# Optimization experiments

Measured on AMD Instinct MI355X. Metric: run time of the kernel, lower is better.

Reference implementation:

```python
import jax, jax.numpy as jnp
import numpy as np

D = 10          # tree depth (perfect binary tree, heap layout)
K = 2           # MAX_CHILD
N = 2 ** D - 1  # nodes per tree = 1023
LD = 256        # latent_dim
B = 128         # batch of trees


def setup_inputs() -> dict:
    key = jax.random.key(0)
    ks = jax.random.split(key, 24)
    p = lambda k, shape: (jax.random.normal(k, shape, jnp.float32) * 0.05)
    return {
        "x_embed": jax.random.normal(ks[0], (B, N, LD), jnp.float32),
        "init_embedding": jax.random.normal(ks[1], (B, LD), jnp.float32),
        # leaf gates cx, ox
        "Wcx": p(ks[2], (LD, LD)), "bcx": p(ks[3], (LD,)),
        "Wox": p(ks[4], (LD, LD)), "box": p(ks[5], (LD,)),
        # token-input gates ix, fx, ux
        "Wix": p(ks[6], (LD, LD)), "bix": p(ks[7], (LD,)),
        "Wfx": p(ks[8], (LD, LD)), "bfx": p(ks[9], (LD,)),
        "Wux": p(ks[10], (LD, LD)), "bux": p(ks[11], (LD,)),
        # per-child gates: i_gates[K], f_gates[K][K], u_gates[K]
        "Wi": p(ks[12], (K, LD, LD)), "bi": p(ks[13], (K, LD)),
        "Wf": p(ks[14], (K, K, LD, LD)), "bf": p(ks[15], (K, K, LD)),
        "Wu": p(ks[16], (K, LD, LD)), "bu": p(ks[17], (K, LD)),
        # output projection oend: Linear(3*latent_dim, latent_dim)
        "Woend": p(ks[18], (3 * LD, LD)), "boend": p(ks[19], (LD,)),
    }


def _tree_lstm(x_embed, Wcx, bcx, Wox, box, Wix, bix, Wfx, bfx, Wux, bux,
               Wi, bi, Wf, bf, Wu, bu):
    lin = lambda x, W, b: x @ W + b
    # --- leaves (deepest level): c = cx(x); h = sigmoid(ox(x)) * tanh(c) ---
    leaf_start = 2 ** (D - 1) - 1
    x_leaf = x_embed[:, leaf_start:]                       # [B, 2^(D-1), d]
    c_leaf = lin(x_leaf, Wcx, bcx)
    h_leaf = jax.nn.sigmoid(lin(x_leaf, Wox, box)) * jnp.tanh(c_leaf)
    c_all = jnp.zeros_like(x_embed).at[:, leaf_start:].set(c_leaf)
    h_all = jnp.zeros_like(x_embed).at[:, leaf_start:].set(h_leaf)
    # --- internal levels, bottom-up (fixed D-1 iterations, vectorized over B*width) ---
    for lvl in range(D - 2, -1, -1):
        s, e = 2 ** lvl - 1, 2 ** (lvl + 1) - 1
        idx = np.arange(s, e)
        ch = np.stack([2 * idx + 1, 2 * idx + 2], axis=1)  # [w, K] heap children
        hch = h_all[:, ch]                                 # [B, w, K, d]
        cch = c_all[:, ch]                                 # [B, w, K, d]
        x = x_embed[:, s:e]                                # [B, w, d]
        # i = sigmoid(ix(x) + sum_k i_gates[k](h_k))
        i = jax.nn.sigmoid(lin(x, Wix, bix)
                           + jnp.einsum('bwkd,kde->bwe', hch, Wi) + bi.sum(0))
        # f_vals[k] = fx(x) + sum_j f_gates[k][j](h_j)   (NO sigmoid, faithful to source)
        f = (lin(x, Wfx, bfx)[:, :, None, :]
             + jnp.einsum('bwjd,kjde->bwke', hch, Wf) + bf.sum(1))   # [B, w, K, d]
        # u = tanh(ux(x) + sum_k u_gates[k](h_k))
        u = jnp.tanh(lin(x, Wux, bux)
                     + jnp.einsum('bwkd,kde->bwe', hch, Wu) + bu.sum(0))
        c = i * u + jnp.sum(f * cch, axis=2)
        h = jnp.tanh(c)
        c_all = c_all.at[:, s:e].set(c)
        h_all = h_all.at[:, s:e].set(h)
    return c_all[:, 0], h_all[:, 0]                        # root state (c, h)


def reference(x_embed, init_embedding, Wcx, bcx, Wox, box, Wix, bix, Wfx, bfx,
              Wux, bux, Wi, bi, Wf, bf, Wu, bu, Woend, boend):
    c_root, h_root = _tree_lstm(x_embed, Wcx, bcx, Wox, box, Wix, bix,
                                Wfx, bfx, Wux, bux, Wi, bi, Wf, bf, Wu, bu)
    s = jnp.concatenate([init_embedding, c_root, h_root], axis=1)  # [B, 3d]
    return jnp.tanh(s @ Woend + boend)                             # [B, d]
```

## Files before the change

### kernel.cpp

```cpp
#include <hip/hip_runtime.h>
#include <hip/hip_bf16.h>
#include <math.h>


#define NNODES 1023
#define BATCH  128
#define LDIM   256

typedef __attribute__((ext_vector_type(8))) short short8;
typedef __attribute__((ext_vector_type(4))) float f32x4;

__device__ __forceinline__ float sigmoidf_(float x) {
    return 1.f / (1.f + expf(-x));
}

__device__ __forceinline__ void split3(float x, ushort& h, ushort& m, ushort& l) {
    unsigned u = __float_as_uint(x);
    unsigned hu = (u + 0x7FFFu + ((u >> 16) & 1u)) & 0xFFFF0000u;
    h = (ushort)(hu >> 16);
    float r = x - __uint_as_float(hu);
    unsigned ur = __float_as_uint(r);
    unsigned mu = (ur + 0x7FFFu + ((ur >> 16) & 1u)) & 0xFFFF0000u;
    m = (ushort)(mu >> 16);
    float r2 = r - __uint_as_float(mu);
    unsigned u2 = __float_as_uint(r2);
    l = (ushort)((u2 + 0x7FFFu + ((u2 >> 16) & 1u)) >> 16);
}

__device__ __forceinline__ unsigned cvt_pk_bf16(float lo, float hi) {
    unsigned r;
    asm("v_cvt_pk_bf16_f32 %0, %1, %2" : "=v"(r) : "v"(lo), "v"(hi));
    return r;
}

struct P3 { unsigned h, m, l; };
__device__ __forceinline__ P3 pack2v(float x0, float x1) {
    P3 p;
    p.h = cvt_pk_bf16(x0, x1);
    float h0 = __uint_as_float(p.h << 16);
    float h1 = __uint_as_float(p.h & 0xFFFF0000u);
    float r0 = x0 - h0, r1 = x1 - h1;
    p.m = cvt_pk_bf16(r0, r1);
    float m0 = __uint_as_float(p.m << 16);
    float m1 = __uint_as_float(p.m & 0xFFFF0000u);
    p.l = cvt_pk_bf16(r0 - m0, r1 - m1);
    return p;
}

__global__ __launch_bounds__(256) void build_weights(
    const float* __restrict__ Wix, const float* __restrict__ bix,
    const float* __restrict__ Wfx, const float* __restrict__ bfx,
    const float* __restrict__ Wux, const float* __restrict__ bux,
    const float* __restrict__ Wi,  const float* __restrict__ bi,
    const float* __restrict__ Wf,  const float* __restrict__ bf,
    const float* __restrict__ Wu,  const float* __restrict__ bu,
    const float* __restrict__ Wcx, const float* __restrict__ bcx,
    const float* __restrict__ Wox, const float* __restrict__ box,
    float* __restrict__ Wbig, float* __restrict__ bias_big,
    float* __restrict__ Wleaf, float* __restrict__ bias_leaf)
{
    int i = blockIdx.x * blockDim.x + threadIdx.x;
    if (i < 768 * 1024) {
        int k = i >> 10, n = i & 1023;
        int g = n >> 8, nn = n & 255;
        float v;
        if (g == 0) {
            v = (k < 256) ? Wix[k * 256 + nn]
              : (k < 512) ? Wi[(k - 256) * 256 + nn]
                          : Wi[65536 + (k - 512) * 256 + nn];
        } else if (g == 1) {
            v = (k < 256) ? Wux[k * 256 + nn]
              : (k < 512) ? Wu[(k - 256) * 256 + nn]
                          : Wu[65536 + (k - 512) * 256 + nn];
        } else {
            int kf = g - 2;
            v = (k < 256) ? Wfx[k * 256 + nn]
              : (k < 512) ? Wf[((kf * 2 + 0) * 256 + (k - 256)) * 256 + nn]
                          : Wf[((kf * 2 + 1) * 256 + (k - 512)) * 256 + nn];
        }
        Wbig[i] = v;
        return;
    }
    i -= 768 * 1024;
    if (i < 1024) {
        int g = i >> 8, nn = i & 255;
        float v;
        if (g == 0)      v = bix[nn] + bi[nn] + bi[256 + nn];
        else if (g == 1) v = bux[nn] + bu[nn] + bu[256 + nn];
        else if (g == 2) v = bfx[nn] + bf[nn] + bf[256 + nn];
        else             v = bfx[nn] + bf[512 + nn] + bf[768 + nn];
        bias_big[i] = v;
        return;
    }
    i -= 1024;
    if (i < 256 * 512) {
        int k = i >> 9, n = i & 511;
        Wleaf[i] = (n < 256) ? Wcx[k * 256 + n] : Wox[k * 256 + (n - 256)];
        return;
    }
    i -= 256 * 512;
    if (i < 512) {
        bias_leaf[i] = (i < 256) ? bcx[i] : box[i - 256];
    }
}

__global__ __launch_bounds__(256) void split_weights_T(
    const float* __restrict__ Wbig,
    ushort* __restrict__ Wth, ushort* __restrict__ Wtm, ushort* __restrict__ Wtl)
{
    __shared__ float sh[32][33];
    const int k0 = blockIdx.x * 32, n0 = blockIdx.y * 32;
    const int t = threadIdx.x;
    {
        int r = t >> 3, c4 = (t & 7) * 4;
        float4 v = *(const float4*)&Wbig[(size_t)(k0 + r) * 1024 + n0 + c4];
        sh[r][c4] = v.x; sh[r][c4 + 1] = v.y; sh[r][c4 + 2] = v.z; sh[r][c4 + 3] = v.w;
    }
    __syncthreads();
    int n = t >> 3, kc = (t & 7) * 4;
    ushort oh[4], om[4], ol[4];
#pragma unroll
    for (int j = 0; j < 4; ++j)
        split3(sh[kc + j][n], oh[j], om[j], ol[j]);
    size_t o = (size_t)(n0 + n) * 768 + k0 + kc;
    *(ushort4*)&Wth[o] = make_ushort4(oh[0], oh[1], oh[2], oh[3]);
    *(ushort4*)&Wtm[o] = make_ushort4(om[0], om[1], om[2], om[3]);
    *(ushort4*)&Wtl[o] = make_ushort4(ol[0], ol[1], ol[2], ol[3]);
}

__global__ __launch_bounds__(256) void split_wleaf_T(
    const float* __restrict__ Wleaf,
    ushort* __restrict__ Lth, ushort* __restrict__ Ltm, ushort* __restrict__ Ltl)
{
    __shared__ float sh[32][33];
    const int k0 = blockIdx.x * 32, n0 = blockIdx.y * 32;
    const int t = threadIdx.x;
    {
        int r = t >> 3, c4 = (t & 7) * 4;
        float4 v = *(const float4*)&Wleaf[(size_t)(k0 + r) * 512 + n0 + c4];
        sh[r][c4] = v.x; sh[r][c4 + 1] = v.y; sh[r][c4 + 2] = v.z; sh[r][c4 + 3] = v.w;
    }
    __syncthreads();
    int n = t >> 3, kc = (t & 7) * 4;
    ushort oh[4], om[4], ol[4];
#pragma unroll
    for (int j = 0; j < 4; ++j)
        split3(sh[kc + j][n], oh[j], om[j], ol[j]);
    size_t o = (size_t)(n0 + n) * 256 + k0 + kc;
    *(ushort4*)&Lth[o] = make_ushort4(oh[0], oh[1], oh[2], oh[3]);
    *(ushort4*)&Ltm[o] = make_ushort4(om[0], om[1], om[2], om[3]);
    *(ushort4*)&Ltl[o] = make_ushort4(ol[0], ol[1], ol[2], ol[3]);
}

__global__ __launch_bounds__(256, 2) void mfma_level_pack(
    const float* __restrict__ x_embed,
    const float* __restrict__ hChild, const float* __restrict__ cChild,
    const ushort* __restrict__ Wth, const ushort* __restrict__ Wtm,
    const ushort* __restrict__ Wtl,
    const float* __restrict__ bias,
    float* __restrict__ hOut, float* __restrict__ cOut, int nstart)
{
    constexpr int AST = 40;
    __shared__ __align__(16) ushort Wlds[3][128 * AST];
    __shared__ __align__(16) ushort Vlds[3][128 * AST];

    const int tid  = threadIdx.x;
    const int node = blockIdx.x;
    const int gy   = blockIdx.y;
    const int lane = tid & 63, wid = tid >> 6;
    const int ni = wid & 1, bw = wid >> 1;
    const int srow = tid & 127, shalf = tid >> 7;

    const float* aX = x_embed + ((size_t)srow * NNODES + (nstart + node)) * LDIM;
    const float* aL = hChild + ((size_t)(2 * node) * BATCH + srow) * LDIM;
    const float* aR = aL + (size_t)BATCH * LDIM;
    const size_t nb = (size_t)(((srow >> 5) << 8) + gy * 32 + (srow & 31)) * 768;
    const ushort* w0 = Wth + nb;
    const ushort* w1 = Wtm + nb;
    const ushort* w2 = Wtl + nb;

    f32x4 acc[4][4];
#pragma unroll
    for (int g = 0; g < 4; ++g)
#pragma unroll
        for (int t2 = 0; t2 < 4; ++t2) acc[g][t2] = (f32x4){0.f, 0.f, 0.f, 0.f};

    float4 a0, a1, a2, a3;
    int4 w00, w01, w10, w11, w20, w21;

#define TREE_LOADS(IT)                                                         \
    {                                                                          \
        const int seg_  = (IT) >> 3;                                           \
        const int koff_ = ((IT) & 7) * 32 + shalf * 16;                        \
        const float* ap_ = (seg_ == 0) ? aX : (seg_ == 1) ? aL : aR;           \
        ap_ += koff_;                                                          \
        a0 = *(const float4*)(ap_);                                            \
        a1 = *(const float4*)(ap_ + 4);                                        \
        a2 = *(const float4*)(ap_ + 8);                                        \
        a3 = *(const float4*)(ap_ + 12);                                       \
        const int bko_ = (IT) * 32 + shalf * 16;                               \
        w00 = *(const int4*)(w0 + bko_); w01 = *(const int4*)(w0 + bko_ + 8);  \
        w10 = *(const int4*)(w1 + bko_); w11 = *(const int4*)(w1 + bko_ + 8);  \
        w20 = *(const int4*)(w2 + bko_); w21 = *(const int4*)(w2 + bko_ + 8);  \
    }

    TREE_LOADS(0);
    for (int it = 0; it < 24; ++it) {
        if (it) __syncthreads();
        {
            P3 p0 = pack2v(a0.x, a0.y), p1 = pack2v(a0.z, a0.w);
            P3 p2 = pack2v(a1.x, a1.y), p3 = pack2v(a1.z, a1.w);
            P3 p4 = pack2v(a2.x, a2.y), p5 = pack2v(a2.z, a2.w);
            P3 p6 = pack2v(a3.x, a3.y), p7 = pack2v(a3.z, a3.w);
            const int base = srow * AST + shalf * 16;
            *(int4*)&Vlds[0][base]     = make_int4((int)p0.h, (int)p1.h, (int)p2.h, (int)p3.h);
            *(int4*)&Vlds[0][base + 8] = make_int4((int)p4.h, (int)p5.h, (int)p6.h, (int)p7.h);
            *(int4*)&Vlds[1][base]     = make_int4((int)p0.m, (int)p1.m, (int)p2.m, (int)p3.m);
            *(int4*)&Vlds[1][base + 8] = make_int4((int)p4.m, (int)p5.m, (int)p6.m, (int)p7.m);
            *(int4*)&Vlds[2][base]     = make_int4((int)p0.l, (int)p1.l, (int)p2.l, (int)p3.l);
            *(int4*)&Vlds[2][base + 8] = make_int4((int)p4.l, (int)p5.l, (int)p6.l, (int)p7.l);
            *(int4*)&Wlds[0][base]     = w00;
            *(int4*)&Wlds[0][base + 8] = w01;
            *(int4*)&Wlds[1][base]     = w10;
            *(int4*)&Wlds[1][base + 8] = w11;
            *(int4*)&Wlds[2][base]     = w20;
            *(int4*)&Wlds[2][base + 8] = w21;
        }
        __syncthreads();
        if (it + 1 < 24) TREE_LOADS(it + 1);
        {
            short8 vf[4][3];
#pragma unroll
            for (int Nt = 0; Nt < 4; ++Nt) {
                const int rb = (bw * 64 + Nt * 16 + (lane & 15)) * AST + (lane >> 4) * 8;
#pragma unroll
                for (int s = 0; s < 3; ++s) vf[Nt][s] = *(const short8*)&Vlds[s][rb];
            }
#pragma unroll
            for (int g = 0; g < 4; ++g) {
                const int cb = (g * 32 + ni * 16 + (lane & 15)) * AST + (lane >> 4) * 8;
                short8 wh = *(const short8*)&Wlds[0][cb];
                short8 wm = *(const short8*)&Wlds[1][cb];
                short8 wl = *(const short8*)&Wlds[2][cb];
#pragma unroll
                for (int Nt = 0; Nt < 4; ++Nt)
                    acc[g][Nt] = __builtin_amdgcn_mfma_f32_16x16x32_bf16(wl, vf[Nt][0], acc[g][Nt], 0, 0, 0);
#pragma unroll
                for (int Nt = 0; Nt < 4; ++Nt)
                    acc[g][Nt] = __builtin_amdgcn_mfma_f32_16x16x32_bf16(wh, vf[Nt][2], acc[g][Nt], 0, 0, 0);
#pragma unroll
                for (int Nt = 0; Nt < 4; ++Nt)
                    acc[g][Nt] = __builtin_amdgcn_mfma_f32_16x16x32_bf16(wm, vf[Nt][1], acc[g][Nt], 0, 0, 0);
#pragma unroll
                for (int Nt = 0; Nt < 4; ++Nt)
                    acc[g][Nt] = __builtin_amdgcn_mfma_f32_16x16x32_bf16(wm, vf[Nt][0], acc[g][Nt], 0, 0, 0);
#pragma unroll
                for (int Nt = 0; Nt < 4; ++Nt)
                    acc[g][Nt] = __builtin_amdgcn_mfma_f32_16x16x32_bf16(wh, vf[Nt][1], acc[g][Nt], 0, 0, 0);
#pragma unroll
                for (int Nt = 0; Nt < 4; ++Nt)
                    acc[g][Nt] = __builtin_amdgcn_mfma_f32_16x16x32_bf16(wh, vf[Nt][0], acc[g][Nt], 0, 0, 0);
            }
        }
    }
#undef TREE_LOADS

    const int nc = gy * 32 + ni * 16 + ((lane >> 4) << 2);
    const size_t cLb = (size_t)(2 * node) * BATCH * LDIM;
    const size_t cRb = cLb + (size_t)BATCH * LDIM;
    const size_t ob  = (size_t)node * BATCH * LDIM;
    const float4 bi4 = *(const float4*)&bias[nc];
    const float4 bu4 = *(const float4*)&bias[256 + nc];
    const float4 b04 = *(const float4*)&bias[512 + nc];
    const float4 b14 = *(const float4*)&bias[768 + nc];
    const float bi_[4] = {bi4.x, bi4.y, bi4.z, bi4.w};
    const float bu_[4] = {bu4.x, bu4.y, bu4.z, bu4.w};
    const float b0_[4] = {b04.x, b04.y, b04.z, b04.w};
    const float b1_[4] = {b14.x, b14.y, b14.z, b14.w};
#pragma unroll
    for (int Nt = 0; Nt < 4; ++Nt) {
        const int b = bw * 64 + Nt * 16 + (lane & 15);
        float4 cL = *(const float4*)&cChild[cLb + (size_t)b * LDIM + nc];
        float4 cR = *(const float4*)&cChild[cRb + (size_t)b * LDIM + nc];
        float cl4[4] = {cL.x, cL.y, cL.z, cL.w};
        float cr4[4] = {cR.x, cR.y, cR.z, cR.w};
        float4 c4, h4;
        float* cp = (float*)&c4; float* hp = (float*)&h4;
#pragma unroll
        for (int j = 0; j < 4; ++j) {
            float gi = sigmoidf_(acc[0][Nt][j] + bi_[j]);
            float gu = tanhf(acc[1][Nt][j] + bu_[j]);
            float f0 = acc[2][Nt][j] + b0_[j];
            float f1 = acc[3][Nt][j] + b1_[j];
            float c  = gi * gu + f0 * cl4[j] + f1 * cr4[j];
            cp[j] = c;
            hp[j] = tanhf(c);
        }
        *(float4*)&cOut[ob + (size_t)b * LDIM + nc] = c4;
        *(float4*)&hOut[ob + (size_t)b * LDIM + nc] = h4;
    }
}

__global__ __launch_bounds__(256, 3) void leaf_mfma(
    const float* __restrict__ x_embed,
    const ushort* __restrict__ Lth, const ushort* __restrict__ Ltm,
    const ushort* __restrict__ Ltl,
    const float* __restrict__ bias_leaf,
    float* __restrict__ hOut, float* __restrict__ cOut)
{
    constexpr int AST = 40;
    __shared__ __align__(16) ushort Wlds[3][64 * AST];
    __shared__ __align__(16) ushort Vlds[3][128 * AST];

    const int tid = threadIdx.x;
    const int ln  = blockIdx.x;
    const int gy  = blockIdx.y;
    const int lane = tid & 63, wid = tid >> 6;
    const int ni = wid & 1, bw = wid >> 1;
    const int srow = tid & 127, shalf = tid >> 7;
    const int wrow = tid & 63, whalf = (tid >> 6) & 1;

    const float* aX = x_embed + ((size_t)srow * NNODES + (511 + ln)) * LDIM;
    const size_t nbw = (size_t)(((wrow >> 5) << 8) + gy * 32 + (wrow & 31)) * 256;
    const ushort* l0 = Lth + nbw;
    const ushort* l1 = Ltm + nbw;
    const ushort* l2 = Ltl + nbw;

    f32x4 acc[2][4];
#pragma unroll
    for (int g = 0; g < 2; ++g)
#pragma unroll
        for (int t2 = 0; t2 < 4; ++t2) acc[g][t2] = (f32x4){0.f, 0.f, 0.f, 0.f};

    float4 a0, a1, a2, a3;
    int4 w00, w01, w10, w11, w20, w21;

#define LEAF_LOADS(IT)                                                         \
    {                                                                          \
        const float* ap_ = aX + (IT) * 32 + shalf * 16;                        \
        a0 = *(const float4*)(ap_);                                            \
        a1 = *(const float4*)(ap_ + 4);                                        \
        a2 = *(const float4*)(ap_ + 8);                                        \
        a3 = *(const float4*)(ap_ + 12);                                       \
        if (tid < 128) {                                                       \
            const int bko_ = (IT) * 32 + whalf * 16;                           \
            w00 = *(const int4*)(l0 + bko_); w01 = *(const int4*)(l0 + bko_ + 8); \
            w10 = *(const int4*)(l1 + bko_); w11 = *(const int4*)(l1 + bko_ + 8); \
            w20 = *(const int4*)(l2 + bko_); w21 = *(const int4*)(l2 + bko_ + 8); \
        }                                                                      \
    }

    LEAF_LOADS(0);
    for (int it = 0; it < 8; ++it) {
        if (it) __syncthreads();
        {
            P3 p0 = pack2v(a0.x, a0.y), p1 = pack2v(a0.z, a0.w);
            P3 p2 = pack2v(a1.x, a1.y), p3 = pack2v(a1.z, a1.w);
            P3 p4 = pack2v(a2.x, a2.y), p5 = pack2v(a2.z, a2.w);
            P3 p6 = pack2v(a3.x, a3.y), p7 = pack2v(a3.z, a3.w);
            const int base = srow * AST + shalf * 16;
            *(int4*)&Vlds[0][base]     = make_int4((int)p0.h, (int)p1.h, (int)p2.h, (int)p3.h);
            *(int4*)&Vlds[0][base + 8] = make_int4((int)p4.h, (int)p5.h, (int)p6.h, (int)p7.h);
            *(int4*)&Vlds[1][base]     = make_int4((int)p0.m, (int)p1.m, (int)p2.m, (int)p3.m);
            *(int4*)&Vlds[1][base + 8] = make_int4((int)p4.m, (int)p5.m, (int)p6.m, (int)p7.m);
            *(int4*)&Vlds[2][base]     = make_int4((int)p0.l, (int)p1.l, (int)p2.l, (int)p3.l);
            *(int4*)&Vlds[2][base + 8] = make_int4((int)p4.l, (int)p5.l, (int)p6.l, (int)p7.l);
            if (tid < 128) {
                const int bw_ = wrow * AST + whalf * 16;
                *(int4*)&Wlds[0][bw_]     = w00;
                *(int4*)&Wlds[0][bw_ + 8] = w01;
                *(int4*)&Wlds[1][bw_]     = w10;
                *(int4*)&Wlds[1][bw_ + 8] = w11;
                *(int4*)&Wlds[2][bw_]     = w20;
                *(int4*)&Wlds[2][bw_ + 8] = w21;
            }
        }
        __syncthreads();
        if (it + 1 < 8) LEAF_LOADS(it + 1);
        {
            short8 vf[4][3];
#pragma unroll
            for (int Nt = 0; Nt < 4; ++Nt) {
                const int rb = (bw * 64 + Nt * 16 + (lane & 15)) * AST + (lane >> 4) * 8;
#pragma unroll
                for (int s = 0; s < 3; ++s) vf[Nt][s] = *(const short8*)&Vlds[s][rb];
            }
#pragma unroll
            for (int g = 0; g < 2; ++g) {
                const int cb = (g * 32 + ni * 16 + (lane & 15)) * AST + (lane >> 4) * 8;
                short8 wh = *(const short8*)&Wlds[0][cb];
                short8 wm = *(const short8*)&Wlds[1][cb];
                short8 wl = *(const short8*)&Wlds[2][cb];
#pragma unroll
                for (int Nt = 0; Nt < 4; ++Nt)
                    acc[g][Nt] = __builtin_amdgcn_mfma_f32_16x16x32_bf16(wl, vf[Nt][0], acc[g][Nt], 0, 0, 0);
#pragma unroll
                for (int Nt = 0; Nt < 4; ++Nt)
                    acc[g][Nt] = __builtin_amdgcn_mfma_f32_16x16x32_bf16(wh, vf[Nt][2], acc[g][Nt], 0, 0, 0);
#pragma unroll
                for (int Nt = 0; Nt < 4; ++Nt)
                    acc[g][Nt] = __builtin_amdgcn_mfma_f32_16x16x32_bf16(wm, vf[Nt][1], acc[g][Nt], 0, 0, 0);
#pragma unroll
                for (int Nt = 0; Nt < 4; ++Nt)
                    acc[g][Nt] = __builtin_amdgcn_mfma_f32_16x16x32_bf16(wm, vf[Nt][0], acc[g][Nt], 0, 0, 0);
#pragma unroll
                for (int Nt = 0; Nt < 4; ++Nt)
                    acc[g][Nt] = __builtin_amdgcn_mfma_f32_16x16x32_bf16(wh, vf[Nt][1], acc[g][Nt], 0, 0, 0);
#pragma unroll
                for (int Nt = 0; Nt < 4; ++Nt)
                    acc[g][Nt] = __builtin_amdgcn_mfma_f32_16x16x32_bf16(wh, vf[Nt][0], acc[g][Nt], 0, 0, 0);
            }
        }
    }
#undef LEAF_LOADS

    const int nc = gy * 32 + ni * 16 + ((lane >> 4) << 2);
    const size_t ob = (size_t)ln * BATCH * LDIM;
    const float4 bc4 = *(const float4*)&bias_leaf[nc];
    const float4 bo4 = *(const float4*)&bias_leaf[256 + nc];
    const float bc_[4] = {bc4.x, bc4.y, bc4.z, bc4.w};
    const float bo_[4] = {bo4.x, bo4.y, bo4.z, bo4.w};
#pragma unroll
    for (int Nt = 0; Nt < 4; ++Nt) {
        const int b = bw * 64 + Nt * 16 + (lane & 15);
        float4 c4, h4;
        float* cp = (float*)&c4; float* hp = (float*)&h4;
#pragma unroll
        for (int j = 0; j < 4; ++j) {
            float c = acc[0][Nt][j] + bc_[j];
            float o = acc[1][Nt][j] + bo_[j];
            cp[j] = c;
            hp[j] = sigmoidf_(o) * tanhf(c);
        }
        size_t po = ob + (size_t)b * LDIM + nc;
        *(float4*)&cOut[po] = c4;
        *(float4*)&hOut[po] = h4;
    }
}

__global__ __launch_bounds__(256) void leaf_kernel(
    const float* __restrict__ x_embed,
    const float* __restrict__ Wleaf, const float* __restrict__ bias_leaf,
    float* __restrict__ hOut, float* __restrict__ cOut)
{
    __shared__ float As[16 * 68];
    __shared__ float Bs[2 * 16 * 64];
    float acc[2][4][4] = {};
    const int tid = threadIdx.x;
    const int ty = tid >> 4, tx = tid & 15;
    const int row0 = blockIdx.x * 64;
    const int n0 = blockIdx.y * 64;
    const int w = row0 >> 7;
    const int ar = tid >> 2;
    const int kq = (tid & 3) * 4;
    const int b = (row0 + ar) & 127;
    const float* xrow = x_embed + ((size_t)b * NNODES + 511 + w) * LDIM;

    for (int k0 = 0; k0 < 256; k0 += 16) {
        float4 av = *(const float4*)(xrow + k0 + kq);
        As[(kq + 0) * 68 + ar] = av.x;
        As[(kq + 1) * 68 + ar] = av.y;
        As[(kq + 2) * 68 + ar] = av.z;
        As[(kq + 3) * 68 + ar] = av.w;
#pragma unroll
        for (int q = 0; q < 2; ++q) {
            int L = q * 256 + tid;
            int g = L >> 8, kk = (L >> 4) & 15, n4 = (L & 15) * 4;
            float4 bv = *(const float4*)(Wleaf + (size_t)(k0 + kk) * 512 + g * 256 + n0 + n4);
            *(float4*)&Bs[(g * 16 + kk) * 64 + n4] = bv;
        }
        __syncthreads();
#pragma unroll
        for (int kk = 0; kk < 16; ++kk) {
            float4 a = *(const float4*)&As[kk * 68 + ty * 4];
            float av4[4] = {a.x, a.y, a.z, a.w};
#pragma unroll
            for (int g = 0; g < 2; ++g) {
                float4 bb = *(const float4*)&Bs[(g * 16 + kk) * 64 + tx * 4];
                float bv4[4] = {bb.x, bb.y, bb.z, bb.w};
#pragma unroll
                for (int ii = 0; ii < 4; ++ii)
#pragma unroll
                    for (int jj = 0; jj < 4; ++jj)
                        acc[g][ii][jj] += av4[ii] * bv4[jj];
            }
        }
        __syncthreads();
    }
#pragma unroll
    for (int ii = 0; ii < 4; ++ii) {
        int r = row0 + ty * 4 + ii;
        int nc = n0 + tx * 4;
        float4 c4, h4;
        float* cp = (float*)&c4; float* hp = (float*)&h4;
#pragma unroll
        for (int jj = 0; jj < 4; ++jj) {
            int n = nc + jj;
            float ac = acc[0][ii][jj] + bias_leaf[n];
            float ao = acc[1][ii][jj] + bias_leaf[256 + n];
            cp[jj] = ac;
            hp[jj] = sigmoidf_(ao) * tanhf(ac);
        }
        *(float4*)&cOut[(size_t)r * LDIM + nc] = c4;
        *(float4*)&hOut[(size_t)r * LDIM + nc] = h4;
    }
}

__global__ __launch_bounds__(256) void level_kernel(
    const float* __restrict__ x_embed,
    const float* __restrict__ hChild, const float* __restrict__ cChild,
    const float* __restrict__ Wbig, const float* __restrict__ bias_big,
    float* __restrict__ hOut, float* __restrict__ cOut,
    int nstart)
{
    __shared__ float As[16 * 68];
    __shared__ float Bs[4 * 16 * 64];
    float acc[4][4][4] = {};
    const int tid = threadIdx.x;
    const int ty = tid >> 4, tx = tid & 15;
    const int row0 = blockIdx.x * 64;
    const int n0 = blockIdx.y * 64;
    const int w = row0 >> 7;
    const int ar = tid >> 2;
    const int kq = (tid & 3) * 4;
    const int b = (row0 + ar) & 127;
    const float* srcX = x_embed + ((size_t)b * NNODES + nstart + w) * LDIM;
    const float* srcL = hChild + ((size_t)(2 * w) * BATCH + b) * LDIM;
    const float* srcR = hChild + ((size_t)(2 * w + 1) * BATCH + b) * LDIM;

    for (int k0 = 0; k0 < 768; k0 += 16) {
        int seg = k0 >> 8, off = k0 & 255;
        const float* src = (seg == 0) ? srcX : (seg == 1) ? srcL : srcR;
        float4 av = *(const float4*)(src + off + kq);
        As[(kq + 0) * 68 + ar] = av.x;
        As[(kq + 1) * 68 + ar] = av.y;
        As[(kq + 2) * 68 + ar] = av.z;
        As[(kq + 3) * 68 + ar] = av.w;
#pragma unroll
        for (int q = 0; q < 4; ++q) {
            int L = q * 256 + tid;
            int g = L >> 8, kk = (L >> 4) & 15, n4 = (L & 15) * 4;
            float4 bv = *(const float4*)(Wbig + (size_t)(k0 + kk) * 1024 + g * 256 + n0 + n4);
            *(float4*)&Bs[(g * 16 + kk) * 64 + n4] = bv;
        }
        __syncthreads();
#pragma unroll
        for (int kk = 0; kk < 16; ++kk) {
            float4 a = *(const float4*)&As[kk * 68 + ty * 4];
            float av4[4] = {a.x, a.y, a.z, a.w};
#pragma unroll
            for (int g = 0; g < 4; ++g) {
                float4 bb = *(const float4*)&Bs[(g * 16 + kk) * 64 + tx * 4];
                float bv4[4] = {bb.x, bb.y, bb.z, bb.w};
#pragma unroll
                for (int ii = 0; ii < 4; ++ii)
#pragma unroll
                    for (int jj = 0; jj < 4; ++jj)
                        acc[g][ii][jj] += av4[ii] * bv4[jj];
            }
        }
        __syncthreads();
    }
    const size_t cLbase = ((size_t)(2 * w) * BATCH) * LDIM;
    const size_t cRbase = ((size_t)(2 * w + 1) * BATCH) * LDIM;
#pragma unroll
    for (int ii = 0; ii < 4; ++ii) {
        int r = row0 + ty * 4 + ii;
        int bb2 = r & 127;
        int nc = n0 + tx * 4;
        float4 cL = *(const float4*)&cChild[cLbase + (size_t)bb2 * LDIM + nc];
        float4 cR = *(const float4*)&cChild[cRbase + (size_t)bb2 * LDIM + nc];
        float cl4[4] = {cL.x, cL.y, cL.z, cL.w};
        float cr4[4] = {cR.x, cR.y, cR.z, cR.w};
        float4 c4, h4;
        float* cp = (float*)&c4; float* hp = (float*)&h4;
#pragma unroll
        for (int jj = 0; jj < 4; ++jj) {
            int n = nc + jj;
            float gi = sigmoidf_(acc[0][ii][jj] + bias_big[n]);
            float gu = tanhf(acc[1][ii][jj] + bias_big[256 + n]);
            float f0 = acc[2][ii][jj] + bias_big[512 + n];
            float f1 = acc[3][ii][jj] + bias_big[768 + n];
            float c = gi * gu + f0 * cl4[jj] + f1 * cr4[jj];
            cp[jj] = c;
            hp[jj] = tanhf(c);
        }
        *(float4*)&cOut[(size_t)r * LDIM + nc] = c4;
        *(float4*)&hOut[(size_t)r * LDIM + nc] = h4;
    }
}

__global__ __launch_bounds__(256) void gemm_part4(
    const float* __restrict__ x_embed, const float* __restrict__ hChild,
    const float* __restrict__ Wbig,
    float* __restrict__ part, int nstart, int rowsTotal)
{
    __shared__ float As[16 * 68];
    __shared__ float Bs[4 * 16 * 64];
    float acc[4][4][4] = {};
    const int tid = threadIdx.x;
    const int ty = tid >> 4, tx = tid & 15;
    const int row0 = blockIdx.x * 64;
    const int n0 = blockIdx.y * 64;
    const int seg = blockIdx.z;
    const int w = row0 >> 7;
    const int ar = tid >> 2;
    const int kq = (tid & 3) * 4;
    const int b = (row0 + ar) & 127;
    const float* src =
        (seg == 0) ? x_embed + ((size_t)b * NNODES + nstart + w) * LDIM
                   : hChild + ((size_t)(2 * w + (seg - 1)) * BATCH + b) * LDIM;

    for (int k0 = 0; k0 < 256; k0 += 16) {
        float4 av = *(const float4*)(src + k0 + kq);
        As[(kq + 0) * 68 + ar] = av.x;
        As[(kq + 1) * 68 + ar] = av.y;
        As[(kq + 2) * 68 + ar] = av.z;
        As[(kq + 3) * 68 + ar] = av.w;
#pragma unroll
        for (int q = 0; q < 4; ++q) {
            int L = q * 256 + tid;
            int g = L >> 8, kk = (L >> 4) & 15, n4 = (L & 15) * 4;
            float4 bv = *(const float4*)(Wbig + (size_t)(seg * 256 + k0 + kk) * 1024
                                         + g * 256 + n0 + n4);
            *(float4*)&Bs[(g * 16 + kk) * 64 + n4] = bv;
        }
        __syncthreads();
#pragma unroll
        for (int kk = 0; kk < 16; ++kk) {
            float4 a = *(const float4*)&As[kk * 68 + ty * 4];
            float av4[4] = {a.x, a.y, a.z, a.w};
#pragma unroll
            for (int g = 0; g < 4; ++g) {
                float4 bb = *(const float4*)&Bs[(g * 16 + kk) * 64 + tx * 4];
                float bv4[4] = {bb.x, bb.y, bb.z, bb.w};
#pragma unroll
                for (int ii = 0; ii < 4; ++ii)
#pragma unroll
                    for (int jj = 0; jj < 4; ++jj)
                        acc[g][ii][jj] += av4[ii] * bv4[jj];
            }
        }
        __syncthreads();
    }
#pragma unroll
    for (int ii = 0; ii < 4; ++ii) {
        int r = row0 + ty * 4 + ii;
        size_t base = ((size_t)seg * rowsTotal + r) * 1024 + n0 + tx * 4;
#pragma unroll
        for (int g = 0; g < 4; ++g)
            *(float4*)&part[base + g * 256] = *(float4*)acc[g][ii];
    }
}

__global__ __launch_bounds__(256) void combine_eps(
    const float* __restrict__ part, const float* __restrict__ cChild,
    const float* __restrict__ bias,
    float* __restrict__ hOut, float* __restrict__ cOut, int rowsTotal)
{
    int idx = blockIdx.x * 256 + threadIdx.x;
    int row = idx >> 6, n = (idx & 63) * 4;
    size_t sseg = (size_t)rowsTotal * 1024;
    const float* p0 = part + (size_t)row * 1024 + n;
    float s[4][4];
#pragma unroll
    for (int g = 0; g < 4; ++g) {
        float4 a = *(const float4*)(p0 + g * 256);
        float4 b = *(const float4*)(p0 + sseg + g * 256);
        float4 c = *(const float4*)(p0 + 2 * sseg + g * 256);
        s[g][0] = a.x + b.x + c.x; s[g][1] = a.y + b.y + c.y;
        s[g][2] = a.z + b.z + c.z; s[g][3] = a.w + b.w + c.w;
    }
    int node = row >> 7, b = row & 127;
    float4 cL = *(const float4*)&cChild[((size_t)(2 * node) * BATCH + b) * LDIM + n];
    float4 cR = *(const float4*)&cChild[((size_t)(2 * node + 1) * BATCH + b) * LDIM + n];
    float cl4[4] = {cL.x, cL.y, cL.z, cL.w};
    float cr4[4] = {cR.x, cR.y, cR.z, cR.w};
    float4 c4, h4;
    float* cp = (float*)&c4; float* hp = (float*)&h4;
#pragma unroll
    for (int jj = 0; jj < 4; ++jj) {
        int nn = n + jj;
        float gi = sigmoidf_(s[0][jj] + bias[nn]);
        float gu = tanhf(s[1][jj] + bias[256 + nn]);
        float f0 = s[2][jj] + bias[512 + nn];
        float f1 = s[3][jj] + bias[768 + nn];
        float c = gi * gu + f0 * cl4[jj] + f1 * cr4[jj];
        cp[jj] = c;
        hp[jj] = tanhf(c);
    }
    *(float4*)&cOut[(size_t)row * LDIM + n] = c4;
    *(float4*)&hOut[(size_t)row * LDIM + n] = h4;
}

__global__ __launch_bounds__(256) void final_kernel(
    const float* __restrict__ init_emb,
    const float* __restrict__ cRoot, const float* __restrict__ hRoot,
    const float* __restrict__ Woend, const float* __restrict__ boend,
    float* __restrict__ out)
{
    __shared__ float sv[768];
    int b = blockIdx.x, t = threadIdx.x;
    sv[t]       = init_emb[(size_t)b * 256 + t];
    sv[256 + t] = cRoot[(size_t)b * 256 + t];
    sv[512 + t] = hRoot[(size_t)b * 256 + t];
    __syncthreads();
    float acc = boend[t];
#pragma unroll 4
    for (int d = 0; d < 768; ++d)
        acc += sv[d] * Woend[(size_t)d * 256 + t];
    out[(size_t)b * 256 + t] = tanhf(acc);
}

extern "C" void kernel_launch(void* const* d_in, const int* in_sizes, int n_in,
                              void* d_out, int out_size, void* d_ws, size_t ws_size,
                              hipStream_t stream)
{
    const float* x_embed  = (const float*)d_in[0];
    const float* init_emb = (const float*)d_in[1];
    const float* Wcx = (const float*)d_in[2];  const float* bcx = (const float*)d_in[3];
    const float* Wox = (const float*)d_in[4];  const float* box = (const float*)d_in[5];
    const float* Wix = (const float*)d_in[6];  const float* bix = (const float*)d_in[7];
    const float* Wfx = (const float*)d_in[8];  const float* bfx = (const float*)d_in[9];
    const float* Wux = (const float*)d_in[10]; const float* bux = (const float*)d_in[11];
    const float* Wi  = (const float*)d_in[12]; const float* bi  = (const float*)d_in[13];
    const float* Wf  = (const float*)d_in[14]; const float* bf  = (const float*)d_in[15];
    const float* Wu  = (const float*)d_in[16]; const float* bu  = (const float*)d_in[17];
    const float* Woend = (const float*)d_in[18]; const float* boend = (const float*)d_in[19];
    float* out = (float*)d_out;
    float* ws  = (float*)d_ws;

    size_t off = 0;
    float* hA = ws + off; off += (size_t)512 * 128 * 256;
    float* cA = ws + off; off += (size_t)512 * 128 * 256;
    float* hB = ws + off; off += (size_t)256 * 128 * 256;
    float* cB = ws + off; off += (size_t)256 * 128 * 256;
    float* Wbig      = ws + off; off += (size_t)768 * 1024;
    float* bias_big  = ws + off; off += 1024;
    float* Wleaf     = ws + off; off += (size_t)256 * 512;
    float* bias_leaf = ws + off; off += 512;
    ushort* Wth = (ushort*)(ws + off); off += (size_t)768 * 1024 / 2;
    ushort* Wtm = (ushort*)(ws + off); off += (size_t)768 * 1024 / 2;
    ushort* Wtl = (ushort*)(ws + off); off += (size_t)768 * 1024 / 2;
    ushort* Lth = (ushort*)(ws + off); off += (size_t)512 * 256 / 2;
    ushort* Ltm = (ushort*)(ws + off); off += (size_t)512 * 256 / 2;
    ushort* Ltl = (ushort*)(ws + off); off += (size_t)512 * 256 / 2;
    size_t mfma_need = off * sizeof(float);
    size_t part_off = off;
    float* part = ws + part_off;

    bool mfma_ok = mfma_need <= ws_size;

    {
        int total = 768 * 1024 + 1024 + 256 * 512 + 512;
        int blocks = (total + 255) / 256;
        build_weights<<<blocks, 256, 0, stream>>>(
            Wix, bix, Wfx, bfx, Wux, bux, Wi, bi, Wf, bf, Wu, bu,
            Wcx, bcx, Wox, box, Wbig, bias_big, Wleaf, bias_leaf);
    }
    if (mfma_ok) {
        split_weights_T<<<dim3(24, 32), 256, 0, stream>>>(Wbig, Wth, Wtm, Wtl);
        split_wleaf_T<<<dim3(8, 16), 256, 0, stream>>>(Wleaf, Lth, Ltm, Ltl);
    }

    if (mfma_ok) {
        leaf_mfma<<<dim3(512, 8), 256, 0, stream>>>(
            x_embed, Lth, Ltm, Ltl, bias_leaf, hA, cA);
    } else {
        leaf_kernel<<<dim3(1024, 4), 256, 0, stream>>>(
            x_embed, Wleaf, bias_leaf, hA, cA);
    }

    float* hbufs[2] = {hA, hB};
    float* cbufs[2] = {cA, cB};
    int child = 0;
    for (int lvl = 8; lvl >= 0; --lvl) {
        int W = 1 << lvl, s = W - 1;
        int outb = child ^ 1;
        size_t rows = (size_t)W * 128;
        bool split = (W <= 16) &&
                     ((part_off + 3 * rows * 1024) * sizeof(float) <= ws_size);
        if (lvl >= 5 && mfma_ok) {
            mfma_level_pack<<<dim3(W, 8), 256, 0, stream>>>(
                x_embed, hbufs[child], cbufs[child], Wth, Wtm, Wtl, bias_big,
                hbufs[outb], cbufs[outb], s);
        } else if (split) {
            gemm_part4<<<dim3(W * 2, 4, 3), 256, 0, stream>>>(
                x_embed, hbufs[child], Wbig, part, s, (int)rows);
            combine_eps<<<(int)(rows / 4), 256, 0, stream>>>(
                part, cbufs[child], bias_big, hbufs[outb], cbufs[outb], (int)rows);
        } else {
            level_kernel<<<dim3(W * 2, 4), 256, 0, stream>>>(
                x_embed, hbufs[child], cbufs[child], Wbig, bias_big,
                hbufs[outb], cbufs[outb], s);
        }
        child = outb;
    }

    final_kernel<<<128, 256, 0, stream>>>(init_emb, cbufs[child], hbufs[child],
                                          Woend, boend, out);
}
```

Measured before the change: 1.088 ms.

## Load activation MFMA fragments directly into registers, dropping activation LDS staging

The internal-level kernel no longer stages the 3-way bf16 split of activations through shared memory. Each wave now loads its own 32 batch rows straight into MFMA B-fragment layout and splits them in registers. The wave work split changes from 2x2 (gate columns x batch) to each wave covering all 128 gate columns for 32 batch rows. This cuts LDS footprint and traffic, which allows 3 blocks per CU instead of 2. The cost is that each wave now does its own split work, and global loads are less coalesced because each lane reads 8 floats from a different row.

```diff
diff --git a/kernel.cpp b/kernel.cpp
--- a/kernel.cpp
+++ b/kernel.cpp
@@ -45,6 +45,17 @@
     float m1 = __uint_as_float(p.m & 0xFFFF0000u);
     p.l = cvt_pk_bf16(r0 - m0, r1 - m1);
     return p;
+}
+
+struct VF { short8 h, m, l; };
+__device__ __forceinline__ VF split8(float4 a, float4 b) {
+    P3 p0 = pack2v(a.x, a.y), p1 = pack2v(a.z, a.w);
+    P3 p2 = pack2v(b.x, b.y), p3 = pack2v(b.z, b.w);
+    VF r;
+    r.h = __builtin_bit_cast(short8, make_uint4(p0.h, p1.h, p2.h, p3.h));
+    r.m = __builtin_bit_cast(short8, make_uint4(p0.m, p1.m, p2.m, p3.m));
+    r.l = __builtin_bit_cast(short8, make_uint4(p0.l, p1.l, p2.l, p3.l));
+    return r;
 }
 
 __global__ __launch_bounds__(256) void build_weights(
@@ -152,7 +163,7 @@
     *(ushort4*)&Ltl[o] = make_ushort4(ol[0], ol[1], ol[2], ol[3]);
 }
 
-__global__ __launch_bounds__(256, 2) void mfma_level_pack(
+__global__ __launch_bounds__(256, 3) void mfma_level_pack(
     const float* __restrict__ x_embed,
     const float* __restrict__ hChild, const float* __restrict__ cChild,
     const ushort* __restrict__ Wth, const ushort* __restrict__ Wtm,
@@ -162,42 +173,47 @@
 {
     constexpr int AST = 40;
     __shared__ __align__(16) ushort Wlds[3][128 * AST];
-    __shared__ __align__(16) ushort Vlds[3][128 * AST];
 
     const int tid  = threadIdx.x;
     const int node = blockIdx.x;
     const int gy   = blockIdx.y;
     const int lane = tid & 63, wid = tid >> 6;
-    const int ni = wid & 1, bw = wid >> 1;
     const int srow = tid & 127, shalf = tid >> 7;
 
-    const float* aX = x_embed + ((size_t)srow * NNODES + (nstart + node)) * LDIM;
-    const float* aL = hChild + ((size_t)(2 * node) * BATCH + srow) * LDIM;
-    const float* aR = aL + (size_t)BATCH * LDIM;
     const size_t nb = (size_t)(((srow >> 5) << 8) + gy * 32 + (srow & 31)) * 768;
     const ushort* w0 = Wth + nb;
     const ushort* w1 = Wtm + nb;
     const ushort* w2 = Wtl + nb;
 
-    f32x4 acc[4][4];
-#pragma unroll
-    for (int g = 0; g < 4; ++g)
-#pragma unroll
-        for (int t2 = 0; t2 < 4; ++t2) acc[g][t2] = (f32x4){0.f, 0.f, 0.f, 0.f};
-
-    float4 a0, a1, a2, a3;
+    const int b0 = wid * 32 + (lane & 15);
+    const int b1 = b0 + 16;
+    const int kl = (lane >> 4) * 8;
+    const float* x0p = x_embed + ((size_t)b0 * NNODES + (nstart + node)) * LDIM + kl;
+    const float* x1p = x_embed + ((size_t)b1 * NNODES + (nstart + node)) * LDIM + kl;
+    const float* l0p = hChild + ((size_t)(2 * node) * BATCH + b0) * LDIM + kl;
+    const float* l1p = hChild + ((size_t)(2 * node) * BATCH + b1) * LDIM + kl;
+    const size_t RSTEP = (size_t)BATCH * LDIM;
+
+    f32x4 acc[8][2];
+#pragma unroll
+    for (int ct = 0; ct < 8; ++ct)
+#pragma unroll
+        for (int t2 = 0; t2 < 2; ++t2) acc[ct][t2] = (f32x4){0.f, 0.f, 0.f, 0.f};
+
+    float4 v00, v01, v10, v11;
     int4 w00, w01, w10, w11, w20, w21;
 
 #define TREE_LOADS(IT)                                                         \
     {                                                                          \
         const int seg_  = (IT) >> 3;                                           \
-        const int koff_ = ((IT) & 7) * 32 + shalf * 16;                        \
-        const float* ap_ = (seg_ == 0) ? aX : (seg_ == 1) ? aL : aR;           \
-        ap_ += koff_;                                                          \
-        a0 = *(const float4*)(ap_);                                            \
-        a1 = *(const float4*)(ap_ + 4);                                        \
-        a2 = *(const float4*)(ap_ + 8);                                        \
-        a3 = *(const float4*)(ap_ + 12);                                       \
+        const int koff_ = ((IT) & 7) * 32;                                     \
+        const float* pa0_ = (seg_ == 0) ? x0p : (seg_ == 1) ? l0p : (l0p + RSTEP); \
+        const float* pa1_ = (seg_ == 0) ? x1p : (seg_ == 1) ? l1p : (l1p + RSTEP); \
+        pa0_ += koff_; pa1_ += koff_;                                          \
+        v00 = *(const float4*)(pa0_);                                          \
+        v01 = *(const float4*)(pa0_ + 4);                                      \
+        v10 = *(const float4*)(pa1_);                                          \
+        v11 = *(const float4*)(pa1_ + 4);                                      \
         const int bko_ = (IT) * 32 + shalf * 16;                               \
         w00 = *(const int4*)(w0 + bko_); w01 = *(const int4*)(w0 + bko_ + 8);  \
         w10 = *(const int4*)(w1 + bko_); w11 = *(const int4*)(w1 + bko_ + 8);  \
@@ -208,17 +224,7 @@
     for (int it = 0; it < 24; ++it) {
         if (it) __syncthreads();
         {
-            P3 p0 = pack2v(a0.x, a0.y), p1 = pack2v(a0.z, a0.w);
-            P3 p2 = pack2v(a1.x, a1.y), p3 = pack2v(a1.z, a1.w);
-            P3 p4 = pack2v(a2.x, a2.y), p5 = pack2v(a2.z, a2.w);
-            P3 p6 = pack2v(a3.x, a3.y), p7 = pack2v(a3.z, a3.w);
             const int base = srow * AST + shalf * 16;
-            *(int4*)&Vlds[0][base]     = make_int4((int)p0.h, (int)p1.h, (int)p2.h, (int)p3.h);
-            *(int4*)&Vlds[0][base + 8] = make_int4((int)p4.h, (int)p5.h, (int)p6.h, (int)p7.h);
-            *(int4*)&Vlds[1][base]     = make_int4((int)p0.m, (int)p1.m, (int)p2.m, (int)p3.m);
-            *(int4*)&Vlds[1][base + 8] = make_int4((int)p4.m, (int)p5.m, (int)p6.m, (int)p7.m);
-            *(int4*)&Vlds[2][base]     = make_int4((int)p0.l, (int)p1.l, (int)p2.l, (int)p3.l);
-            *(int4*)&Vlds[2][base + 8] = make_int4((int)p4.l, (int)p5.l, (int)p6.l, (int)p7.l);
             *(int4*)&Wlds[0][base]     = w00;
             *(int4*)&Wlds[0][base + 8] = w01;
             *(int4*)&Wlds[1][base]     = w10;
@@ -227,77 +233,67 @@
             *(int4*)&Wlds[2][base + 8] = w21;
         }
         __syncthreads();
+        VF f0 = split8(v00, v01);
+        VF f1 = split8(v10, v11);
         if (it + 1 < 24) TREE_LOADS(it + 1);
-        {
-            short8 vf[4][3];
-#pragma unroll
-            for (int Nt = 0; Nt < 4; ++Nt) {
-                const int rb = (bw * 64 + Nt * 16 + (lane & 15)) * AST + (lane >> 4) * 8;
-#pragma unroll
-                for (int s = 0; s < 3; ++s) vf[Nt][s] = *(const short8*)&Vlds[s][rb];
-            }
-#pragma unroll
-            for (int g = 0; g < 4; ++g) {
-                const int cb = (g * 32 + ni * 16 + (lane & 15)) * AST + (lane >> 4) * 8;
-                short8 wh = *(const short8*)&Wlds[0][cb];
-                short8 wm = *(const short8*)&Wlds[1][cb];
-                short8 wl = *(const short8*)&Wlds[2][cb];
-#pragma unroll
-                for (int Nt = 0; Nt < 4; ++Nt)
-                    acc[g][Nt] = __builtin_amdgcn_mfma_f32_16x16x32_bf16(wl, vf[Nt][0], acc[g][Nt], 0, 0, 0);
-#pragma unroll
-                for (int Nt = 0; Nt < 4; ++Nt)
-                    acc[g][Nt] = __builtin_amdgcn_mfma_f32_16x16x32_bf16(wh, vf[Nt][2], acc[g][Nt], 0, 0, 0);
-#pragma unroll
-                for (int Nt = 0; Nt < 4; ++Nt)
-                    acc[g][Nt] = __builtin_amdgcn_mfma_f32_16x16x32_bf16(wm, vf[Nt][1], acc[g][Nt], 0, 0, 0);
-#pragma unroll
-                for (int Nt = 0; Nt < 4; ++Nt)
-                    acc[g][Nt] = __builtin_amdgcn_mfma_f32_16x16x32_bf16(wm, vf[Nt][0], acc[g][Nt], 0, 0, 0);
-#pragma unroll
-                for (int Nt = 0; Nt < 4; ++Nt)
-                    acc[g][Nt] = __builtin_amdgcn_mfma_f32_16x16x32_bf16(wh, vf[Nt][1], acc[g][Nt], 0, 0, 0);
-#pragma unroll
-                for (int Nt = 0; Nt < 4; ++Nt)
-                    acc[g][Nt] = __builtin_amdgcn_mfma_f32_16x16x32_bf16(wh, vf[Nt][0], acc[g][Nt], 0, 0, 0);
-            }
+#pragma unroll
+        for (int ct = 0; ct < 8; ++ct) {
+            const int cb = (ct * 16 + (lane & 15)) * AST + (lane >> 4) * 8;
+            short8 wh = *(const short8*)&Wlds[0][cb];
+            short8 wm = *(const short8*)&Wlds[1][cb];
+            short8 wl = *(const short8*)&Wlds[2][cb];
+            acc[ct][0] = __builtin_amdgcn_mfma_f32_16x16x32_bf16(wl, f0.h, acc[ct][0], 0, 0, 0);
+            acc[ct][1] = __builtin_amdgcn_mfma_f32_16x16x32_bf16(wl, f1.h, acc[ct][1], 0, 0, 0);
+            acc[ct][0] = __builtin_amdgcn_mfma_f32_16x16x32_bf16(wh, f0.l, acc[ct][0], 0, 0, 0);
+            acc[ct][1] = __builtin_amdgcn_mfma_f32_16x16x32_bf16(wh, f1.l, acc[ct][1], 0, 0, 0);
+            acc[ct][0] = __builtin_amdgcn_mfma_f32_16x16x32_bf16(wm, f0.m, acc[ct][0], 0, 0, 0);
+            acc[ct][1] = __builtin_amdgcn_mfma_f32_16x16x32_bf16(wm, f1.m, acc[ct][1], 0, 0, 0);
+            acc[ct][0] = __builtin_amdgcn_mfma_f32_16x16x32_bf16(wm, f0.h, acc[ct][0], 0, 0, 0);
+            acc[ct][1] = __builtin_amdgcn_mfma_f32_16x16x32_bf16(wm, f1.h, acc[ct][1], 0, 0, 0);
+            acc[ct][0] = __builtin_amdgcn_mfma_f32_16x16x32_bf16(wh, f0.m, acc[ct][0], 0, 0, 0);
+            acc[ct][1] = __builtin_amdgcn_mfma_f32_16x16x32_bf16(wh, f1.m, acc[ct][1], 0, 0, 0);
+            acc[ct][0] = __builtin_amdgcn_mfma_f32_16x16x32_bf16(wh, f0.h, acc[ct][0], 0, 0, 0);
+            acc[ct][1] = __builtin_amdgcn_mfma_f32_16x16x32_bf16(wh, f1.h, acc[ct][1], 0, 0, 0);
         }
     }
 #undef TREE_LOADS
 
-    const int nc = gy * 32 + ni * 16 + ((lane >> 4) << 2);
     const size_t cLb = (size_t)(2 * node) * BATCH * LDIM;
     const size_t cRb = cLb + (size_t)BATCH * LDIM;
     const size_t ob  = (size_t)node * BATCH * LDIM;
-    const float4 bi4 = *(const float4*)&bias[nc];
-    const float4 bu4 = *(const float4*)&bias[256 + nc];
-    const float4 b04 = *(const float4*)&bias[512 + nc];
-    const float4 b14 = *(const float4*)&bias[768 + nc];
-    const float bi_[4] = {bi4.x, bi4.y, bi4.z, bi4.w};
-    const float bu_[4] = {bu4.x, bu4.y, bu4.z, bu4.w};
-    const float b0_[4] = {b04.x, b04.y, b04.z, b04.w};
-    const float b1_[4] = {b14.x, b14.y, b14.z, b14.w};
-#pragma unroll
-    for (int Nt = 0; Nt < 4; ++Nt) {
-        const int b = bw * 64 + Nt * 16 + (lane & 15);
-        float4 cL = *(const float4*)&cChild[cLb + (size_t)b * LDIM + nc];
-        float4 cR = *(const float4*)&cChild[cRb + (size_t)b * LDIM + nc];
-        float cl4[4] = {cL.x, cL.y, cL.z, cL.w};
-        float cr4[4] = {cR.x, cR.y, cR.z, cR.w};
-        float4 c4, h4;
-        float* cp = (float*)&c4; float* hp = (float*)&h4;
-#pragma unroll
-        for (int j = 0; j < 4; ++j) {
-            float gi = sigmoidf_(acc[0][Nt][j] + bi_[j]);
-            float gu = tanhf(acc[1][Nt][j] + bu_[j]);
-            float f0 = acc[2][Nt][j] + b0_[j];
-            float f1 = acc[3][Nt][j] + b1_[j];
-            float c  = gi * gu + f0 * cl4[j] + f1 * cr4[j];
-            cp[j] = c;
-            hp[j] = tanhf(c);
-        }
-        *(float4*)&cOut[ob + (size_t)b * LDIM + nc] = c4;
-        *(float4*)&hOut[ob + (size_t)b * LDIM + nc] = h4;
+#pragma unroll
+    for (int half = 0; half < 2; ++half) {
+        const int nc = gy * 32 + half * 16 + ((lane >> 4) << 2);
+        const float4 bi4 = *(const float4*)&bias[nc];
+        const float4 bu4 = *(const float4*)&bias[256 + nc];
+        const float4 b04 = *(const float4*)&bias[512 + nc];
+        const float4 b14 = *(const float4*)&bias[768 + nc];
+        const float bi_[4] = {bi4.x, bi4.y, bi4.z, bi4.w};
+        const float bu_[4] = {bu4.x, bu4.y, bu4.z, bu4.w};
+        const float b0_[4] = {b04.x, b04.y, b04.z, b04.w};
+        const float b1_[4] = {b14.x, b14.y, b14.z, b14.w};
+#pragma unroll
+        for (int Nt = 0; Nt < 2; ++Nt) {
+            const int b = wid * 32 + Nt * 16 + (lane & 15);
+            float4 cL = *(const float4*)&cChild[cLb + (size_t)b * LDIM + nc];
+            float4 cR = *(const float4*)&cChild[cRb + (size_t)b * LDIM + nc];
+            float cl4[4] = {cL.x, cL.y, cL.z, cL.w};
+            float cr4[4] = {cR.x, cR.y, cR.z, cR.w};
+            float4 c4, h4;
+            float* cp = (float*)&c4; float* hp = (float*)&h4;
+#pragma unroll
+            for (int j = 0; j < 4; ++j) {
+                float gi = sigmoidf_(acc[0 + half][Nt][j] + bi_[j]);
+                float gu = tanhf(acc[2 + half][Nt][j] + bu_[j]);
+                float f0 = acc[4 + half][Nt][j] + b0_[j];
+                float f1 = acc[6 + half][Nt][j] + b1_[j];
+                float c  = gi * gu + f0 * cl4[j] + f1 * cr4[j];
+                cp[j] = c;
+                hp[j] = tanhf(c);
+            }
+            *(float4*)&cOut[ob + (size_t)b * LDIM + nc] = c4;
+            *(float4*)&hOut[ob + (size_t)b * LDIM + nc] = h4;
+        }
     }
 }
 
```

Measured after the change: 1.080 ms. Within noise of the previous version (-0.7%).
